# Kernel optimization log

Measured on AMD Instinct MI355X. Metric: run time of the kernel, lower is better.

## Reference

```python
import jax, jax.numpy as jnp
import numpy as np

NUM_GENES = 4000
NUM_PATCHES = 64
EMBED_DIM = 192
NUM_CELLS = 4096


def setup_inputs() -> dict:
    key = jax.random.key(0)
    k1, k2, k3, k4 = jax.random.split(key, 4)
    x = jax.random.normal(k1, (NUM_CELLS, NUM_GENES), dtype=jnp.float32)
    # binary gene->pathway membership mask [num_genes, num_patches]
    mask = jax.random.randint(k2, (NUM_GENES, NUM_PATCHES), 0, 2).astype(jnp.float32)
    W = jax.random.normal(k3, (NUM_GENES, NUM_PATCHES * EMBED_DIM), dtype=jnp.float32) * 0.02
    b = jax.random.normal(k4, (NUM_PATCHES * EMBED_DIM,), dtype=jnp.float32) * 0.02
    return {"x": x, "mask": mask, "W": W, "b": b}


def reference(x, mask, W, b):
    # Expand mask as in __init__: np.repeat(mask, embed_dim, axis=1)
    # -> column j belongs to pathway j // embed_dim.
    mask_rep = jnp.repeat(mask, EMBED_DIM, axis=1)  # [genes, patches*embed]
    # CustomizedLinear: dense matmul with statically masked weight.
    out = x @ (W * mask_rep) + b  # [cells, patches*embed]
    # rearrange 'h (w c) -> h c w' with c = num_patches
    out = out.reshape(NUM_CELLS, EMBED_DIM, NUM_PATCHES).transpose(0, 2, 1)
    # norm_layer=None -> Identity
    return out  # [cells, num_patches, embed_dim]
```

## Files before the change

kernel.cpp:

```cpp
#include <hip/hip_runtime.h>
#include <hip/hip_bf16.h>

#define M_CELLS 4096
#define N_GENES 4000
#define KP      4032
#define NKT     63
#define N_OUT   12288
#define EMB     192
#define NPATCH  64

#define BM 256
#define BN 256
#define BK 64
#define BTILE (BN * BK)

typedef __attribute__((ext_vector_type(8))) short bf16x8_t;
typedef __attribute__((ext_vector_type(8))) unsigned short u16x8_t;
typedef __attribute__((ext_vector_type(4))) float f32x4_t;

__device__ __forceinline__ unsigned short f2bf(float f) {
  __hip_bfloat16 h = __float2bfloat16(f);
  return *reinterpret_cast<unsigned short*>(&h);
}

__device__ __forceinline__ void gll16(const unsigned short* g, unsigned short* l) {
  __builtin_amdgcn_global_load_lds(
      (const __attribute__((address_space(1))) void*)g,
      (__attribute__((address_space(3))) void*)l, 16, 0, 0);
}

__global__ __launch_bounds__(256) void prep_fused(const float* __restrict__ x,
                                                  const float* __restrict__ mask,
                                                  const float* __restrict__ W,
                                                  unsigned short* __restrict__ A,
                                                  unsigned short* __restrict__ Bt) {
  __shared__ unsigned short sT[256 * 64];
  const int t = threadIdx.x;
  if (blockIdx.x < 1024) {
    const int NG = M_CELLS * (KP / 8);
    for (int g = blockIdx.x * 256 + t; g < NG; g += 1024 * 256) {
      int row = g / (KP / 8);
      int kc  = g - row * (KP / 8);
      int k   = kc * 8;
      u16x8_t v;
      if (k < N_GENES) {
        float4 f0 = *reinterpret_cast<const float4*>(x + (size_t)row * N_GENES + k);
        float4 f1 = *reinterpret_cast<const float4*>(x + (size_t)row * N_GENES + k + 4);
        v[0] = f2bf(f0.x); v[1] = f2bf(f0.y); v[2] = f2bf(f0.z); v[3] = f2bf(f0.w);
        v[4] = f2bf(f1.x); v[5] = f2bf(f1.y); v[6] = f2bf(f1.z); v[7] = f2bf(f1.w);
      } else {
        v = (u16x8_t)0;
      }
      *reinterpret_cast<u16x8_t*>(A + (size_t)row * KP + k) = v;
    }
  } else {
    const int idx = blockIdx.x - 1024;
    const int jb  = idx % 48;
    const int kt  = idx / 48;
    const int j   = jb * 256 + t;
    const int pw  = j / EMB;
#pragma unroll
    for (int ch = 0; ch < 8; ++ch) {
      u16x8_t v;
#pragma unroll
      for (int u = 0; u < 8; ++u) {
        int kg = kt * 64 + ch * 8 + u;
        float val = 0.f;
        if (kg < N_GENES) val = W[(size_t)kg * N_OUT + j] * mask[kg * NPATCH + pw];
        v[u] = f2bf(val);
      }
      *reinterpret_cast<u16x8_t*>(&sT[t * 64 + ((ch ^ (t & 7)) * 8)]) = v;
    }
    __syncthreads();
#pragma unroll
    for (int it = 0; it < 8; ++it) {
      int f  = it * 256 + t;
      int p  = f >> 5, u = f & 31;
      int el = u >> 3;
      int r  = el * 64 + p;
      u16x8_t v = *reinterpret_cast<const u16x8_t*>(&sT[r * 64 + (((u & 7) ^ (r & 7)) * 8)]);
      int jp0 = p * EMB + jb * 4;
      int nt  = jp0 >> 8, c = jp0 & 255;
      *reinterpret_cast<u16x8_t*>(&Bt[(size_t)(nt * NKT + kt) * BTILE + (size_t)c * 64 + u * 8]) = v;
    }
  }
}

#define ABASE(buf, ks) (((buf) * 2 + (ks)) * 8192)
#define BBASE(buf, ks) (32768 + ((buf) * 2 + (ks)) * 8192)

__global__ __launch_bounds__(512, 2) void gemm_bf16(const unsigned short* __restrict__ A,
                                                    const unsigned short* __restrict__ Bt,
                                                    const float* __restrict__ bias,
                                                    float* __restrict__ out) {
  __shared__ unsigned short lds[65536];

  const int tid  = threadIdx.x;
  const int lane = tid & 63;
  const int wid  = tid >> 6;
  const int wm   = wid >> 2;
  const int wn   = wid & 3;
  const int lr   = lane & 15;
  const int hi   = lane >> 4;
  const int swz  = (lr >> 1) & 3;

  const int bid = blockIdx.x;
  const int xcd = bid & 7;
  const int l   = bid >> 3;
  const int mt  = l & 15;
  const int nt  = xcd * 6 + (l >> 4);
  const int m0  = mt * BM;
  const int n0  = nt * BN;

  const int aoff = (wm * 128 + lr) * 32 + ((hi ^ swz) << 3);
  const int boff = (wn * 64 + lr) * 32 + ((hi ^ swz) << 3);

  const int srow = tid >> 2;
  const int ssl  = ((tid & 3) ^ ((tid >> 3) & 3)) << 3;
  const unsigned short* aS0 = A + (size_t)(m0 + srow) * KP + ssl;
  const unsigned short* aS1 = aS0 + (size_t)128 * KP;
  const unsigned short* bS0 = Bt + (size_t)nt * NKT * BTILE + (size_t)srow * 64 + ssl;
  const unsigned short* bS1 = bS0 + 8192;

#define STAGE_A(kt, kh, buf) { \
    gll16(aS0 + (kt) * 64 + (kh) * 32, &lds[ABASE(buf, kh) + tid * 8]); \
    gll16(aS1 + (kt) * 64 + (kh) * 32, &lds[ABASE(buf, kh) + 4096 + tid * 8]); }
#define STAGE_B(kt, kh, buf) { \
    gll16(bS0 + (size_t)(kt) * BTILE + (kh) * 32, &lds[BBASE(buf, kh) + tid * 8]); \
    gll16(bS1 + (size_t)(kt) * BTILE + (kh) * 32, &lds[BBASE(buf, kh) + 4096 + tid * 8]); }

#define RD_PA(buf, ks) { \
    af[0] = *reinterpret_cast<const bf16x8_t*>(&lds[ABASE(buf, ks) + aoff]); \
    _Pragma("unroll") for (int n_ = 0; n_ < 4; ++n_) \
      bfr[n_] = *reinterpret_cast<const bf16x8_t*>(&lds[BBASE(buf, ks) + boff + n_ * 512]); \
    _Pragma("unroll") for (int m_ = 1; m_ < 4; ++m_) \
      af[m_] = *reinterpret_cast<const bf16x8_t*>(&lds[ABASE(buf, ks) + aoff + m_ * 512]); }
#define RD_PB(buf, ks) \
    _Pragma("unroll") for (int m_ = 0; m_ < 4; ++m_) \
      af[m_] = *reinterpret_cast<const bf16x8_t*>(&lds[ABASE(buf, ks) + aoff + (4 + m_) * 512]);

#define MM16(mh) \
    __builtin_amdgcn_s_setprio(1); \
    _Pragma("unroll") for (int m_ = 0; m_ < 4; ++m_) \
    _Pragma("unroll") for (int n_ = 0; n_ < 4; ++n_) \
      acc[(mh) * 4 + m_][n_] = __builtin_amdgcn_mfma_f32_16x16x32_bf16( \
          af[m_], bfr[n_], acc[(mh) * 4 + m_][n_], 0, 0, 0); \
    __builtin_amdgcn_s_setprio(0);

#define SFENCE() asm volatile("" ::: "memory")
#define SYNC8() \
    asm volatile("s_waitcnt vmcnt(8) lgkmcnt(0)" ::: "memory"); \
    __builtin_amdgcn_s_barrier(); SFENCE()
#define SYNC4() \
    asm volatile("s_waitcnt vmcnt(4) lgkmcnt(0)" ::: "memory"); \
    __builtin_amdgcn_s_barrier(); SFENCE()

  f32x4_t acc[8][4] = {};
  bf16x8_t af[4], bfr[4];

  STAGE_A(0, 0, 0); STAGE_B(0, 0, 0);
  STAGE_A(0, 1, 0); STAGE_B(0, 1, 0);
  STAGE_A(1, 0, 1); STAGE_B(1, 0, 1);
  asm volatile("s_waitcnt vmcnt(8)" ::: "memory");
  __builtin_amdgcn_s_barrier();
  SFENCE();

  for (int i = 0; i < 31; ++i) {
    const int tb = 2 * i + 1, tc = 2 * i + 2;
    const int td = (tb + 2 <= 62) ? tb + 2 : 62;

    RD_PA(0, 0); STAGE_A(tb, 1, 1); SYNC8(); MM16(0);
    RD_PB(0, 0); STAGE_B(tb, 1, 1); SYNC8(); MM16(1);
    RD_PA(0, 1); STAGE_A(tc, 0, 0); SYNC8(); MM16(0);
    RD_PB(0, 1); STAGE_B(tc, 0, 0); SYNC8(); MM16(1);
    RD_PA(1, 0); STAGE_A(tc, 1, 0); SYNC8(); MM16(0);
    RD_PB(1, 0); STAGE_B(tc, 1, 0); SYNC8(); MM16(1);
    RD_PA(1, 1); STAGE_A(td, 0, 1); SYNC8(); MM16(0);
    RD_PB(1, 1); STAGE_B(td, 0, 1); SYNC8(); MM16(1);
  }

  RD_PA(0, 0); MM16(0);
  RD_PB(0, 0); MM16(1);
  SYNC4();
  RD_PA(0, 1); MM16(0);
  RD_PB(0, 1); MM16(1);
  asm volatile("s_waitcnt vmcnt(0)" ::: "memory");
  __builtin_amdgcn_s_barrier();

#pragma unroll
  for (int n = 0; n < 4; ++n) {
    int jc = n0 + wn * 64 + n * 16 + lr;
    float bv = bias[(jc % EMB) * NPATCH + (jc / EMB)];
#pragma unroll
    for (int m = 0; m < 8; ++m) {
      int row = m0 + wm * 128 + m * 16 + hi * 4;
      float* o = out + (size_t)row * N_OUT + jc;
#pragma unroll
      for (int r = 0; r < 4; ++r)
        o[(size_t)r * N_OUT] = acc[m][n][r] + bv;
    }
  }
}

__global__ __launch_bounds__(256) void fallback_gemm(const float* __restrict__ x,
                                                     const float* __restrict__ mask,
                                                     const float* __restrict__ W,
                                                     const float* __restrict__ b,
                                                     float* __restrict__ out) {
  __shared__ float sX[64 * 33];
  __shared__ float sB2[32 * 65];
  const int t  = threadIdx.x;
  const int c0 = blockIdx.x * 64;
  const int j0 = blockIdx.y * 64;
  const int tr = t >> 4, tc = t & 15;
  float acc[4][4] = {};
  for (int k0 = 0; k0 < N_GENES; k0 += 32) {
    __syncthreads();
#pragma unroll
    for (int i = 0; i < 8; ++i) {
      int f = i * 256 + t;
      int row = f >> 5, kk = f & 31;
      sX[row * 33 + kk] = x[(size_t)(c0 + row) * N_GENES + k0 + kk];
    }
#pragma unroll
    for (int i = 0; i < 8; ++i) {
      int f = i * 256 + t;
      int kk = f >> 6, cl = f & 63;
      int jp = j0 + cl;
      int jorig = (jp % EMB) * NPATCH + jp / EMB;
      sB2[kk * 65 + cl] = W[(size_t)(k0 + kk) * N_OUT + jorig] * mask[(k0 + kk) * NPATCH + jorig / EMB];
    }
    __syncthreads();
#pragma unroll
    for (int kk = 0; kk < 32; ++kk) {
      float a[4], bb[4];
#pragma unroll
      for (int r = 0; r < 4; ++r) a[r] = sX[(tr * 4 + r) * 33 + kk];
#pragma unroll
      for (int c = 0; c < 4; ++c) bb[c] = sB2[kk * 65 + tc * 4 + c];
#pragma unroll
      for (int r = 0; r < 4; ++r)
#pragma unroll
        for (int c = 0; c < 4; ++c) acc[r][c] += a[r] * bb[c];
    }
  }
#pragma unroll
  for (int r = 0; r < 4; ++r)
#pragma unroll
    for (int c = 0; c < 4; ++c) {
      int jp = j0 + tc * 4 + c;
      int jorig = (jp % EMB) * NPATCH + jp / EMB;
      out[(size_t)(c0 + tr * 4 + r) * N_OUT + jp] = acc[r][c] + b[jorig];
    }
}

extern "C" void kernel_launch(void* const* d_in, const int* in_sizes, int n_in,
                              void* d_out, int out_size, void* d_ws, size_t ws_size,
                              hipStream_t stream) {
  const float* x    = (const float*)d_in[0];
  const float* mask = (const float*)d_in[1];
  const float* W    = (const float*)d_in[2];
  const float* b    = (const float*)d_in[3];
  float* out = (float*)d_out;

  const size_t needA = (size_t)M_CELLS * KP * sizeof(unsigned short);
  const size_t needB = (size_t)N_OUT * KP * sizeof(unsigned short);

  if (ws_size >= needA + needB) {
    unsigned short* Abf = (unsigned short*)d_ws;
    unsigned short* Bt  = (unsigned short*)((char*)d_ws + needA);
    prep_fused<<<4048, 256, 0, stream>>>(x, mask, W, Abf, Bt);
    gemm_bf16<<<768, 512, 0, stream>>>(Abf, Bt, b, out);
  } else {
    fallback_gemm<<<dim3(64, 192), 256, 0, stream>>>(x, mask, W, b, out);
  }
}
```

Measured before the change: 485.7 us.

## Restructure GEMM k-loop barriers and vectorize masked-weight prep loads

The GEMM main loop now issues both A and B stage loads for a slot up front, then runs both M-halves of MFMAs using separate A-fragment registers. It synchronizes once per k-half instead of twice, cutting barrier count and lgkmcnt waits per iteration. The weight-prep path now reads W with float4 loads, keeps mask values in shared memory, and uses a padded, re-swizzled LDS transpose tile. The extra fragment registers raise VGPR pressure under the 512×2 launch bound, which could cause spills or lower occupancy.

```diff
diff --git a/kernel.cpp b/kernel.cpp
--- a/kernel.cpp
+++ b/kernel.cpp
@@ -34,7 +34,8 @@
                                                   const float* __restrict__ W,
                                                   unsigned short* __restrict__ A,
                                                   unsigned short* __restrict__ Bt) {
-  __shared__ unsigned short sT[256 * 64];
+  __shared__ unsigned short sT[256 * 72];
+  __shared__ float smask[256];
   const int t = threadIdx.x;
   if (blockIdx.x < 1024) {
     const int NG = M_CELLS * (KP / 8);
@@ -57,30 +58,62 @@
     const int idx = blockIdx.x - 1024;
     const int jb  = idx % 48;
     const int kt  = idx / 48;
-    const int j   = jb * 256 + t;
-    const int pw  = j / EMB;
-#pragma unroll
-    for (int ch = 0; ch < 8; ++ch) {
-      u16x8_t v;
-#pragma unroll
-      for (int u = 0; u < 8; ++u) {
-        int kg = kt * 64 + ch * 8 + u;
-        float val = 0.f;
-        if (kg < N_GENES) val = W[(size_t)kg * N_OUT + j] * mask[kg * NPATCH + pw];
-        v[u] = f2bf(val);
+    const int q   = t & 63;
+    const int o   = t >> 6;
+    const int pwbase = (jb * 256) / EMB;
+    {
+      const int kg_l = t & 63;
+      const int pwi  = t >> 6;
+      const int kg   = kt * 64 + kg_l;
+      const int pw   = pwbase + pwi;
+      float mv = 0.f;
+      if (kg < N_GENES && pw < NPATCH) mv = mask[kg * NPATCH + pw];
+      smask[kg_l * 4 + pwi] = mv;
+    }
+    __syncthreads();
+    const int jbase = jb * 256 + q * 4;
+    int pwi_[4];
+#pragma unroll
+    for (int dj = 0; dj < 4; ++dj) pwi_[dj] = (jbase + dj) / EMB - pwbase;
+
+    u16x8_t hreg[4][2];
+#pragma unroll
+    for (int hb = 0; hb < 2; ++hb) {
+#pragma unroll
+      for (int kk8 = 0; kk8 < 8; ++kk8) {
+        const int kk = hb * 8 + kk8;
+        const int kg = kt * 64 + o * 16 + kk;
+        float4 f;
+        if (kg < N_GENES) f = *reinterpret_cast<const float4*>(W + (size_t)kg * N_OUT + jbase);
+        else              f = make_float4(0.f, 0.f, 0.f, 0.f);
+        const float fv[4] = {f.x, f.y, f.z, f.w};
+#pragma unroll
+        for (int dj = 0; dj < 4; ++dj) {
+          float m = smask[(o * 16 + kk) * 4 + pwi_[dj]];
+          hreg[dj][hb][kk8] = f2bf(fv[dj] * m);
+        }
       }
-      *reinterpret_cast<u16x8_t*>(&sT[t * 64 + ((ch ^ (t & 7)) * 8)]) = v;
+    }
+#pragma unroll
+    for (int dj = 0; dj < 4; ++dj) {
+      const int jl = q * 4 + dj;
+#pragma unroll
+      for (int hb = 0; hb < 2; ++hb) {
+        const int s = (o * 2 + hb) ^ ((jl >> 2) & 7) ^ ((jl >> 5) & 7);
+        *reinterpret_cast<u16x8_t*>(&sT[jl * 72 + s * 8]) = hreg[dj][hb];
+      }
     }
     __syncthreads();
 #pragma unroll
     for (int it = 0; it < 8; ++it) {
-      int f  = it * 256 + t;
-      int p  = f >> 5, u = f & 31;
-      int el = u >> 3;
-      int r  = el * 64 + p;
-      u16x8_t v = *reinterpret_cast<const u16x8_t*>(&sT[r * 64 + (((u & 7) ^ (r & 7)) * 8)]);
-      int jp0 = p * EMB + jb * 4;
-      int nt  = jp0 >> 8, c = jp0 & 255;
+      const int f  = it * 256 + t;
+      const int p  = f >> 5, u = f & 31;
+      const int el = u >> 3;
+      const int r  = el * 64 + p;
+      const int s  = (u & 7) ^ ((r >> 2) & 7) ^ ((r >> 5) & 7);
+      u16x8_t v = *reinterpret_cast<const u16x8_t*>(&sT[r * 72 + s * 8]);
+      const int jp0 = p * EMB + jb * 4;
+      const int nt  = jp0 >> 8, c = jp0 & 255;
       *reinterpret_cast<u16x8_t*>(&Bt[(size_t)(nt * NKT + kt) * BTILE + (size_t)c * 64 + u * 8]) = v;
     }
   }
@@ -130,60 +163,68 @@
     gll16(bS1 + (size_t)(kt) * BTILE + (kh) * 32, &lds[BBASE(buf, kh) + 4096 + tid * 8]); }
 
 #define RD_PA(buf, ks) { \
-    af[0] = *reinterpret_cast<const bf16x8_t*>(&lds[ABASE(buf, ks) + aoff]); \
+    afA[0] = *reinterpret_cast<const bf16x8_t*>(&lds[ABASE(buf, ks) + aoff]); \
     _Pragma("unroll") for (int n_ = 0; n_ < 4; ++n_) \
       bfr[n_] = *reinterpret_cast<const bf16x8_t*>(&lds[BBASE(buf, ks) + boff + n_ * 512]); \
     _Pragma("unroll") for (int m_ = 1; m_ < 4; ++m_) \
-      af[m_] = *reinterpret_cast<const bf16x8_t*>(&lds[ABASE(buf, ks) + aoff + m_ * 512]); }
+      afA[m_] = *reinterpret_cast<const bf16x8_t*>(&lds[ABASE(buf, ks) + aoff + m_ * 512]); }
 #define RD_PB(buf, ks) \
     _Pragma("unroll") for (int m_ = 0; m_ < 4; ++m_) \
-      af[m_] = *reinterpret_cast<const bf16x8_t*>(&lds[ABASE(buf, ks) + aoff + (4 + m_) * 512]);
-
-#define MM16(mh) \
+      afB[m_] = *reinterpret_cast<const bf16x8_t*>(&lds[ABASE(buf, ks) + aoff + (4 + m_) * 512]);
+
+#define MM16A() \
     __builtin_amdgcn_s_setprio(1); \
     _Pragma("unroll") for (int m_ = 0; m_ < 4; ++m_) \
     _Pragma("unroll") for (int n_ = 0; n_ < 4; ++n_) \
-      acc[(mh) * 4 + m_][n_] = __builtin_amdgcn_mfma_f32_16x16x32_bf16( \
-          af[m_], bfr[n_], acc[(mh) * 4 + m_][n_], 0, 0, 0); \
+      acc[m_][n_] = __builtin_amdgcn_mfma_f32_16x16x32_bf16(afA[m_], bfr[n_], acc[m_][n_], 0, 0, 0); \
     __builtin_amdgcn_s_setprio(0);
-
-#define SFENCE() asm volatile("" ::: "memory")
-#define SYNC8() \
-    asm volatile("s_waitcnt vmcnt(8) lgkmcnt(0)" ::: "memory"); \
-    __builtin_amdgcn_s_barrier(); SFENCE()
-#define SYNC4() \
-    asm volatile("s_waitcnt vmcnt(4) lgkmcnt(0)" ::: "memory"); \
-    __builtin_amdgcn_s_barrier(); SFENCE()
+#define MM16B() \
+    __builtin_amdgcn_s_setprio(1); \
+    _Pragma("unroll") for (int m_ = 0; m_ < 4; ++m_) \
+    _Pragma("unroll") for (int n_ = 0; n_ < 4; ++n_) \
+      acc[4 + m_][n_] = __builtin_amdgcn_mfma_f32_16x16x32_bf16(afB[m_], bfr[n_], acc[4 + m_][n_], 0, 0, 0); \
+    __builtin_amdgcn_s_setprio(0);
+
+#define VMBAR(N) \
+    asm volatile("s_waitcnt vmcnt(" #N ")" ::: "memory"); \
+    __builtin_amdgcn_s_barrier(); \
+    asm volatile("" ::: "memory")
 
   f32x4_t acc[8][4] = {};
-  bf16x8_t af[4], bfr[4];
+  bf16x8_t afA[4], afB[4], bfr[4];
 
   STAGE_A(0, 0, 0); STAGE_B(0, 0, 0);
   STAGE_A(0, 1, 0); STAGE_B(0, 1, 0);
   STAGE_A(1, 0, 1); STAGE_B(1, 0, 1);
-  asm volatile("s_waitcnt vmcnt(8)" ::: "memory");
-  __builtin_amdgcn_s_barrier();
-  SFENCE();
+  VMBAR(8);
 
   for (int i = 0; i < 31; ++i) {
     const int tb = 2 * i + 1, tc = 2 * i + 2;
     const int td = (tb + 2 <= 62) ? tb + 2 : 62;
 
-    RD_PA(0, 0); STAGE_A(tb, 1, 1); SYNC8(); MM16(0);
-    RD_PB(0, 0); STAGE_B(tb, 1, 1); SYNC8(); MM16(1);
-    RD_PA(0, 1); STAGE_A(tc, 0, 0); SYNC8(); MM16(0);
-    RD_PB(0, 1); STAGE_B(tc, 0, 0); SYNC8(); MM16(1);
-    RD_PA(1, 0); STAGE_A(tc, 1, 0); SYNC8(); MM16(0);
-    RD_PB(1, 0); STAGE_B(tc, 1, 0); SYNC8(); MM16(1);
-    RD_PA(1, 1); STAGE_A(td, 0, 1); SYNC8(); MM16(0);
-    RD_PB(1, 1); STAGE_B(td, 0, 1); SYNC8(); MM16(1);
-  }
-
-  RD_PA(0, 0); MM16(0);
-  RD_PB(0, 0); MM16(1);
-  SYNC4();
-  RD_PA(0, 1); MM16(0);
-  RD_PB(0, 1); MM16(1);
+    STAGE_A(tb, 1, 1); STAGE_B(tb, 1, 1);
+    RD_PA(0, 0); MM16A();
+    RD_PB(0, 0); MM16B();
+    VMBAR(8);
+    STAGE_A(tc, 0, 0); STAGE_B(tc, 0, 0);
+    RD_PA(0, 1); MM16A();
+    RD_PB(0, 1); MM16B();
+    VMBAR(8);
+    STAGE_A(tc, 1, 0); STAGE_B(tc, 1, 0);
+    RD_PA(1, 0); MM16A();
+    RD_PB(1, 0); MM16B();
+    VMBAR(8);
+    STAGE_A(td, 0, 1); STAGE_B(td, 0, 1);
+    RD_PA(1, 1); MM16A();
+    RD_PB(1, 1); MM16B();
+    VMBAR(8);
+  }
+
+  RD_PA(0, 0); MM16A();
+  RD_PB(0, 0); MM16B();
+  VMBAR(4);
+  RD_PA(0, 1); MM16A();
+  RD_PB(0, 1); MM16B();
   asm volatile("s_waitcnt vmcnt(0)" ::: "memory");
   __builtin_amdgcn_s_barrier();
 
```

Result: faster. 428.0 us, median of 2 (-11.9%).
